# Kernel tuning notes

Measured on AMD Instinct MI355X. Metric: run time of the kernel, lower is better.

The kernel has to match this reference:

```python
import jax, jax.numpy as jnp
import numpy as np

H = 8  # heads

def setup_inputs() -> dict:
    key = jax.random.key(0)
    k0, k1, k2, k3 = jax.random.split(key, 4)
    B, L, D = 4, 1024, 512
    K = jax.random.normal(k0, (B, L, D), dtype=jnp.float32)
    Q = jax.random.normal(k1, (B, L, D), dtype=jnp.float32)
    V = jax.random.normal(k2, (B, L, D), dtype=jnp.float32)
    # realistic padding: each doc has a valid length in [L/2, L]
    lengths = jax.random.randint(k3, (B,), L // 2, L + 1)
    pos = jnp.arange(L)
    valid = pos[None, :] < lengths[:, None]          # [B, L]
    pad_mask = valid[:, :, None] & valid[:, None, :]  # [B, L, L]
    bx_packed = ~valid                                # [B, L] True where padded
    doc_sizes = lengths.astype(jnp.float32)[:, None]  # [B, 1]
    gamma = jnp.ones((H,), dtype=jnp.float32)   # LayerNorm(heads) weight
    beta = jnp.zeros((H,), dtype=jnp.float32)   # LayerNorm(heads) bias
    return {"K": K, "Q": Q, "V": V, "doc_sizes": doc_sizes,
            "gamma": gamma, "beta": beta,
            "pad_mask": pad_mask, "bx_packed": bx_packed}


def reference(K, Q, V, doc_sizes, gamma, beta, pad_mask, bx_packed):
    B, L, D = K.shape
    d = D // H
    split = lambda x: x.reshape(B, L, H, d).transpose(0, 2, 1, 3)  # [B,H,L,d]
    k, q, v = split(K), split(Q), split(V)

    # InnerMatrix: inner-product similarity -> [B,H,L,L]
    cw = jnp.einsum('bhld,bhmd->bhlm', k, q)

    # LayerNorm over heads axis (torch views [B,H,L*L] -> [B,L*L,H], LN over H)
    mu = cw.mean(axis=1, keepdims=True)
    var = cw.var(axis=1, keepdims=True)
    cw = (cw - mu) / jnp.sqrt(var + 1e-5)
    cw = cw * gamma[None, :, None, None] + beta[None, :, None, None]
    # leaky = -1.0 default: float(leaky > 0) == 0, leaky-relu branch is a no-op

    # masked softmax over keys, NaN (fully-masked rows) -> 0
    cw = jnp.where(pad_mask[:, None, :, :], cw, -jnp.inf)
    cw = jax.nn.softmax(cw, axis=-1)
    cw = jnp.where(jnp.isnan(cw), 0.0, cw)

    # aggregated per-token weights: sum over queries, mean over heads -> [B,L]
    w = cw.sum(axis=-2).mean(axis=1)
    w = w / doc_sizes
    w = jnp.where(bx_packed, -jnp.inf, w)
    w = jax.nn.softmax(w, axis=-1)
    w = jnp.where(jnp.isnan(w), 0.0, w)

    # weighted V aggregation, merge heads back -> [B,L,D]
    out = jnp.einsum('bhlm,bhmd->bhld', cw, v)
    out = out.transpose(0, 2, 1, 3).reshape(B, L, D)
    return out, w[..., None]
```

## Files before the change

kernel.cpp:

```cpp
#include <hip/hip_runtime.h>
#include <math.h>

#define L_ 1024
#define D_ 512

typedef _Float16 half8 __attribute__((ext_vector_type(8)));
typedef _Float16 half4v __attribute__((ext_vector_type(4)));
typedef _Float16 half2v __attribute__((ext_vector_type(2)));
typedef float floatx4 __attribute__((ext_vector_type(4)));

#define LDS_PITCH 264

__global__ __launch_bounds__(256) void prep(
    const float* __restrict__ K, const float* __restrict__ Q,
    const float* __restrict__ V,
    _Float16* __restrict__ K16, _Float16* __restrict__ Q16,
    _Float16* __restrict__ Vt)
{
    __shared__ _Float16 tile[64][72];
    const int t = threadIdx.x;
    const int bi = blockIdx.x;
    if (bi < 256) {
        for (int it = 0; it < 16; ++it) {
            size_t f = (size_t)bi * 4096 + it * 256 + t;
            const float4* src; _Float16* dst;
            if (f < 524288) { src = (const float4*)K; dst = K16; }
            else            { src = (const float4*)Q; dst = Q16; f -= 524288; }
            float4 v = src[f];
            half4v h = { (_Float16)v.x, (_Float16)v.y, (_Float16)v.z, (_Float16)v.w };
            *(half4v*)&dst[f * 4] = h;
        }
    } else {
        const int id = bi - 256;
        const int mt = id & 15, h = (id >> 4) & 7, b = id >> 7;
        const float4* Vf4 = (const float4*)V;
        for (int it = 0; it < 4; ++it) {
            const int ml = (t >> 4) + 16 * it;
            const int c4 = t & 15;
            float4 v = Vf4[(size_t)(b * 1024 + mt * 64 + ml) * 128 + h * 16 + c4];
            tile[c4 * 4 + 0][ml] = (_Float16)v.x;
            tile[c4 * 4 + 1][ml] = (_Float16)v.y;
            tile[c4 * 4 + 2][ml] = (_Float16)v.z;
            tile[c4 * 4 + 3][ml] = (_Float16)v.w;
        }
        __syncthreads();
        const int d = t >> 2, seg = t & 3;
        half8 o0 = *(half8*)&tile[d][seg * 16];
        half8 o1 = *(half8*)&tile[d][seg * 16 + 8];
        size_t obase = ((size_t)(b * 8 + h) * 64 + d) * 1024 + mt * 64 + seg * 16;
        *(half8*)&Vt[obase] = o0;
        *(half8*)&Vt[obase + 8] = o1;
    }
}

__global__ __launch_bounds__(256) void qk_ln(
    const _Float16* __restrict__ K16, const _Float16* __restrict__ Q16,
    const float* __restrict__ gamma, const float* __restrict__ beta,
    const float* __restrict__ doc,
    _Float16* __restrict__ S, float* __restrict__ spart)
{
    __shared__ _Float16 se[8 * 16 * LDS_PITCH];

    const int t  = threadIdx.x;
    const int bi = blockIdx.x;
    const int b  = bi & 3;
    const int lt = (bi >> 2) & 63;
    const int q  = bi >> 8;
    const int wv = t >> 6, lane = t & 63;
    const int col = lane & 15, quad = lane >> 4;
    const int len = (int)doc[b];
    const int lbase = lt * 16;

    float g[8], be[8], M = 0.f;
    #pragma unroll
    for (int h = 0; h < 8; ++h) {
        g[h] = gamma[h]; be[h] = beta[h];
        M = fmaxf(M, 2.8285f * fabsf(g[h]) + fabsf(be[h]));
    }

    const _Float16* Kb = K16 + (size_t)b * 524288;
    const _Float16* Qb = Q16 + (size_t)b * 524288;
    const size_t krow = (size_t)(lbase + col) * 512;

    half8 a0[8], a1[8];
    #pragma unroll
    for (int h = 0; h < 8; ++h) {
        a0[h] = *(const half8*)&Kb[krow + h * 64 + quad * 8];
        a1[h] = *(const half8*)&Kb[krow + h * 64 + 32 + quad * 8];
    }

    float sum[8][4];
    #pragma unroll
    for (int h = 0; h < 8; ++h)
        #pragma unroll
        for (int r = 0; r < 4; ++r) sum[h][r] = 0.f;

    for (int mt = 0; mt < 4; ++mt) {
        const int m0 = q * 256 + wv * 64 + mt * 16;
        const size_t qrow = (size_t)(m0 + col) * 512;
        floatx4 c[8];
        #pragma unroll
        for (int h = 0; h < 8; ++h) {
            half8 b0 = *(const half8*)&Qb[qrow + h * 64 + quad * 8];
            half8 b1 = *(const half8*)&Qb[qrow + h * 64 + 32 + quad * 8];
            floatx4 z = {0.f, 0.f, 0.f, 0.f};
            z    = __builtin_amdgcn_mfma_f32_16x16x32_f16(a0[h], b0, z, 0, 0, 0);
            c[h] = __builtin_amdgcn_mfma_f32_16x16x32_f16(a1[h], b1, c[h] = z, 0, 0, 0);
        }
        const bool mok = (m0 + col) < len;
        #pragma unroll
        for (int r = 0; r < 4; ++r) {
            const int l = lbase + quad * 4 + r;
            float mu = 0.f;
            #pragma unroll
            for (int h = 0; h < 8; ++h) mu += c[h][r];
            mu *= 0.125f;
            float var = 0.f;
            #pragma unroll
            for (int h = 0; h < 8; ++h) { float dd = c[h][r] - mu; var += dd * dd; }
            var *= 0.125f;
            const float rs = 1.0f / sqrtf(var + 1e-5f);
            const bool keep = mok && (l < len);
            #pragma unroll
            for (int h = 0; h < 8; ++h) {
                float e = 0.f;
                if (keep) {
                    float val = (c[h][r] - mu) * rs * g[h] + be[h];
                    e = __expf(val - M);
                }
                sum[h][r] += e;
                se[(h * 16 + quad * 4 + r) * LDS_PITCH + wv * 64 + mt * 16 + col] =
                    (_Float16)e;
            }
        }
    }

    #pragma unroll
    for (int h = 0; h < 8; ++h)
        #pragma unroll
        for (int r = 0; r < 4; ++r) {
            float s = sum[h][r];
            s += __shfl_xor(s, 1); s += __shfl_xor(s, 2);
            s += __shfl_xor(s, 4); s += __shfl_xor(s, 8);
            sum[h][r] = s;
        }
    if (col == 0) {
        #pragma unroll
        for (int h = 0; h < 8; ++h)
            #pragma unroll
            for (int r = 0; r < 4; ++r)
                spart[((size_t)((b * 8 + h) * 1024 + lbase + quad * 4 + r)) * 16
                      + q * 4 + wv] = sum[h][r];
    }
    __syncthreads();

    for (int it = 0; it < 16; ++it) {
        const int rr = it * 8 + (t >> 5);
        const int h = rr >> 4, l = rr & 15;
        half8 v = *(half8*)&se[rr * LDS_PITCH + (t & 31) * 8];
        *(half8*)&S[((size_t)((b * 8 + h) * 1024 + lbase + l)) * 1024
                    + q * 256 + (t & 31) * 8] = v;
    }
}

__global__ __launch_bounds__(256) void stats_reduce(
    const float* __restrict__ spart, const float* __restrict__ doc,
    float* __restrict__ inv)
{
    const int i = blockIdx.x * 256 + threadIdx.x;
    const int l = i & 1023;
    const int b = i >> 13;
    const int len = (int)doc[b];
    float s = 0.f;
    #pragma unroll
    for (int j = 0; j < 16; ++j) s += spart[(size_t)i * 16 + j];
    inv[i] = (l < len && s > 0.f) ? 1.0f / s : 0.f;
}

__global__ __launch_bounds__(256) void pv(
    const _Float16* __restrict__ S, const _Float16* __restrict__ Vt,
    const float* __restrict__ invp,
    float* __restrict__ out, float* __restrict__ wacc)
{
    __shared__ float cs[1024];
    const int t = threadIdx.x, wv = t >> 6, lane = t & 63;
    const int col = lane & 15, quad = lane >> 4;
    const int bi = blockIdx.x;
    const int lb = bi & 15, h = (bi >> 4) & 7, b = bi >> 7;
    const int l0 = lb * 64 + wv * 16;

    #pragma unroll
    for (int i = 0; i < 4; ++i) cs[t + 256 * i] = 0.f;
    __syncthreads();

    const _Float16* Arow = S + ((size_t)(b * 8 + h) * 1024 + l0 + col) * 1024;
    const _Float16* Vb = Vt + (size_t)(b * 8 + h) * 65536;
    const float inv = invp[(size_t)(b * 8 + h) * 1024 + l0 + col];

    floatx4 acc[4] = {{0,0,0,0},{0,0,0,0},{0,0,0,0},{0,0,0,0}};
    for (int kc = 0; kc < 32; ++kc) {
        const int m0 = kc * 32 + quad * 8;
        half8 e = *(const half8*)&Arow[m0];
        half8 a;
        #pragma unroll
        for (int j = 0; j < 8; ++j) a[j] = (_Float16)((float)e[j] * inv);

        #pragma unroll
        for (int u = 0; u < 4; ++u) {
            half2v p2 = { a[2 * u], a[2 * u + 1] };
            int bits = *(int*)&p2;
            #pragma unroll
            for (int o = 1; o < 16; o <<= 1) {
                int ob = __shfl_xor(bits, o);
                half2v po = *(half2v*)&ob;
                half2v pc = *(half2v*)&bits;
                pc[0] = pc[0] + po[0]; pc[1] = pc[1] + po[1];
                bits = *(int*)&pc;
            }
            if (col == 0) {
                half2v pc = *(half2v*)&bits;
                atomicAdd(&cs[m0 + 2 * u],     (float)pc[0]);
                atomicAdd(&cs[m0 + 2 * u + 1], (float)pc[1]);
            }
        }
        #pragma unroll
        for (int dt = 0; dt < 4; ++dt) {
            half8 bf = *(const half8*)&Vb[(size_t)(dt * 16 + col) * 1024 + m0];
            acc[dt] = __builtin_amdgcn_mfma_f32_16x16x32_f16(a, bf, acc[dt], 0, 0, 0);
        }
    }
    #pragma unroll
    for (int r = 0; r < 4; ++r) {
        const int l = l0 + quad * 4 + r;
        float* orow = out + (size_t)(b * 1024 + l) * 512 + h * 64;
        #pragma unroll
        for (int dt = 0; dt < 4; ++dt)
            orow[dt * 16 + col] = acc[dt][r];
    }
    __syncthreads();
    #pragma unroll
    for (int i = 0; i < 4; ++i) {
        const int m = t + 256 * i;
        atomicAdd(&wacc[b * 1024 + m], cs[m]);
    }
}

__global__ __launch_bounds__(256) void w_final(
    const float* __restrict__ wacc, const float* __restrict__ doc,
    float* __restrict__ wout)
{
    const int b = blockIdx.x;
    const int t = threadIdx.x;
    __shared__ float red[4];

    const float ds = doc[b];
    const int len = (int)ds;

    float v[4];
    float mx = -INFINITY;
    #pragma unroll
    for (int i = 0; i < 4; ++i) {
        const int m = t + 256 * i;
        const float raw = wacc[b * L_ + m];
        v[i] = (m < len) ? (raw * 0.125f) / ds : -INFINITY;
        mx = fmaxf(mx, v[i]);
    }
    #pragma unroll
    for (int off = 1; off < 64; off <<= 1) mx = fmaxf(mx, __shfl_xor(mx, off));
    if ((t & 63) == 0) red[t >> 6] = mx;
    __syncthreads();
    mx = fmaxf(fmaxf(red[0], red[1]), fmaxf(red[2], red[3]));

    float e[4];
    float sm = 0.f;
    #pragma unroll
    for (int i = 0; i < 4; ++i) {
        e[i] = (v[i] != -INFINITY) ? __expf(v[i] - mx) : 0.f;
        sm += e[i];
    }
    #pragma unroll
    for (int off = 1; off < 64; off <<= 1) sm += __shfl_xor(sm, off);
    __syncthreads();
    if ((t & 63) == 0) red[t >> 6] = sm;
    __syncthreads();
    sm = red[0] + red[1] + red[2] + red[3];
    const float inv = (sm > 0.f) ? 1.0f / sm : 0.f;

    #pragma unroll
    for (int i = 0; i < 4; ++i)
        wout[b * L_ + t + 256 * i] = e[i] * inv;
}

extern "C" void kernel_launch(void* const* d_in, const int* in_sizes, int n_in,
                              void* d_out, int out_size, void* d_ws, size_t ws_size,
                              hipStream_t stream)
{
    const float* K     = (const float*)d_in[0];
    const float* Q     = (const float*)d_in[1];
    const float* V     = (const float*)d_in[2];
    const float* doc   = (const float*)d_in[3];
    const float* gamma = (const float*)d_in[4];
    const float* beta  = (const float*)d_in[5];

    float* out  = (float*)d_out;
    float* wout = out + (size_t)4 * L_ * D_;

    _Float16* S    = (_Float16*)d_ws;
    _Float16* K16  = S + (size_t)33554432;
    _Float16* Q16  = K16 + 2097152;
    _Float16* Vt   = Q16 + 2097152;
    float*    spart = (float*)(Vt + 2097152);
    float*    invp  = spart + 524288;
    float*    wacc  = invp + 32768;

    hipMemsetAsync(wacc, 0, 4096 * sizeof(float), stream);
    prep        <<<dim3(768),  dim3(256), 0, stream>>>(K, Q, V, K16, Q16, Vt);
    qk_ln       <<<dim3(1024), dim3(256), 0, stream>>>(K16, Q16, gamma, beta, doc, S, spart);
    stats_reduce<<<dim3(128),  dim3(256), 0, stream>>>(spart, doc, invp);
    pv          <<<dim3(512),  dim3(256), 0, stream>>>(S, Vt, invp, out, wacc);
    w_final     <<<dim3(4),    dim3(256), 0, stream>>>(wacc, doc, wout);
}
```

Baseline: 201.8 us.

## Split column-sum out of PV kernel and apply row normalization post-MFMA

The PV kernel no longer normalizes each probability before the MFMA, and no longer computes the per-key column sums with shuffle reductions and LDS atomics. Row normalization is instead applied once to the accumulated output, since scaling a row commutes with the product. A register ring buffer prefetches the S rows eight chunks ahead. A separate wsum kernel re-reads S to compute the column sums with global atomics, which costs an extra pass over the 64MB fp16 score matrix in exchange for a much leaner MFMA loop.

```diff
diff --git a/kernel.cpp b/kernel.cpp
--- a/kernel.cpp
+++ b/kernel.cpp
@@ -180,69 +180,75 @@
 __global__ __launch_bounds__(256) void pv(
     const _Float16* __restrict__ S, const _Float16* __restrict__ Vt,
     const float* __restrict__ invp,
-    float* __restrict__ out, float* __restrict__ wacc)
-{
-    __shared__ float cs[1024];
+    float* __restrict__ out)
+{
     const int t = threadIdx.x, wv = t >> 6, lane = t & 63;
     const int col = lane & 15, quad = lane >> 4;
     const int bi = blockIdx.x;
     const int lb = bi & 15, h = (bi >> 4) & 7, b = bi >> 7;
     const int l0 = lb * 64 + wv * 16;
 
-    #pragma unroll
-    for (int i = 0; i < 4; ++i) cs[t + 256 * i] = 0.f;
-    __syncthreads();
-
     const _Float16* Arow = S + ((size_t)(b * 8 + h) * 1024 + l0 + col) * 1024;
     const _Float16* Vb = Vt + (size_t)(b * 8 + h) * 65536;
-    const float inv = invp[(size_t)(b * 8 + h) * 1024 + l0 + col];
 
     floatx4 acc[4] = {{0,0,0,0},{0,0,0,0},{0,0,0,0},{0,0,0,0}};
+
+    half8 ebuf[8];
+    #pragma unroll
+    for (int i = 0; i < 8; ++i)
+        ebuf[i] = *(const half8*)&Arow[i * 32 + quad * 8];
+
+    #pragma unroll
     for (int kc = 0; kc < 32; ++kc) {
-        const int m0 = kc * 32 + quad * 8;
-        half8 e = *(const half8*)&Arow[m0];
-        half8 a;
-        #pragma unroll
-        for (int j = 0; j < 8; ++j) a[j] = (_Float16)((float)e[j] * inv);
-
-        #pragma unroll
-        for (int u = 0; u < 4; ++u) {
-            half2v p2 = { a[2 * u], a[2 * u + 1] };
-            int bits = *(int*)&p2;
-            #pragma unroll
-            for (int o = 1; o < 16; o <<= 1) {
-                int ob = __shfl_xor(bits, o);
-                half2v po = *(half2v*)&ob;
-                half2v pc = *(half2v*)&bits;
-                pc[0] = pc[0] + po[0]; pc[1] = pc[1] + po[1];
-                bits = *(int*)&pc;
-            }
-            if (col == 0) {
-                half2v pc = *(half2v*)&bits;
-                atomicAdd(&cs[m0 + 2 * u],     (float)pc[0]);
-                atomicAdd(&cs[m0 + 2 * u + 1], (float)pc[1]);
-            }
-        }
+        half8 a = ebuf[kc & 7];
+        if (kc + 8 < 32)
+            ebuf[kc & 7] = *(const half8*)&Arow[(kc + 8) * 32 + quad * 8];
         #pragma unroll
         for (int dt = 0; dt < 4; ++dt) {
-            half8 bf = *(const half8*)&Vb[(size_t)(dt * 16 + col) * 1024 + m0];
+            half8 bf = *(const half8*)&Vb[(size_t)(dt * 16 + col) * 1024
+                                          + kc * 32 + quad * 8];
             acc[dt] = __builtin_amdgcn_mfma_f32_16x16x32_f16(a, bf, acc[dt], 0, 0, 0);
         }
     }
+
     #pragma unroll
     for (int r = 0; r < 4; ++r) {
         const int l = l0 + quad * 4 + r;
+        const float ivr = invp[(size_t)(b * 8 + h) * 1024 + l];
         float* orow = out + (size_t)(b * 1024 + l) * 512 + h * 64;
         #pragma unroll
         for (int dt = 0; dt < 4; ++dt)
-            orow[dt * 16 + col] = acc[dt][r];
-    }
-    __syncthreads();
-    #pragma unroll
-    for (int i = 0; i < 4; ++i) {
-        const int m = t + 256 * i;
-        atomicAdd(&wacc[b * 1024 + m], cs[m]);
-    }
+            orow[dt * 16 + col] = acc[dt][r] * ivr;
+    }
+}
+
+__global__ __launch_bounds__(256) void wsum(
+    const _Float16* __restrict__ S, const float* __restrict__ invp,
+    float* __restrict__ wacc)
+{
+    const int t = threadIdx.x;
+    const int bi = blockIdx.x;
+    const int lc = bi & 15, h = (bi >> 4) & 7, b = bi >> 7;
+    const size_t rbase = (size_t)(b * 8 + h) * 1024 + lc * 64;
+    const _Float16* Sb = S + rbase * 1024;
+    const float* ivb = invp + rbase;
+    const int m0 = t * 4;
+
+    float a0 = 0.f, a1 = 0.f, a2 = 0.f, a3 = 0.f;
+    #pragma unroll 8
+    for (int l = 0; l < 64; ++l) {
+        const float iv = ivb[l];
+        half4v e = *(const half4v*)&Sb[(size_t)l * 1024 + m0];
+        a0 += (float)e[0] * iv;
+        a1 += (float)e[1] * iv;
+        a2 += (float)e[2] * iv;
+        a3 += (float)e[3] * iv;
+    }
+    float* wb = wacc + b * 1024 + m0;
+    atomicAdd(&wb[0], a0);
+    atomicAdd(&wb[1], a1);
+    atomicAdd(&wb[2], a2);
+    atomicAdd(&wb[3], a3);
 }
 
 __global__ __launch_bounds__(256) void w_final(
@@ -317,6 +323,7 @@
     prep        <<<dim3(768),  dim3(256), 0, stream>>>(K, Q, V, K16, Q16, Vt);
     qk_ln       <<<dim3(1024), dim3(256), 0, stream>>>(K16, Q16, gamma, beta, doc, S, spart);
     stats_reduce<<<dim3(128),  dim3(256), 0, stream>>>(spart, doc, invp);
-    pv          <<<dim3(512),  dim3(256), 0, stream>>>(S, Vt, invp, out, wacc);
+    pv          <<<dim3(512),  dim3(256), 0, stream>>>(S, Vt, invp, out);
+    wsum        <<<dim3(512),  dim3(256), 0, stream>>>(S, invp, wacc);
     w_final     <<<dim3(4),    dim3(256), 0, stream>>>(wacc, doc, wout);
 }
```

After: 209.7 us. 1.04x slower.
